# Kernel optimization log

Measured on AMD Instinct MI355X. Metric: run time of the kernel, lower is better.

Reference implementation:

```python
import jax, jax.numpy as jnp
import numpy as np

B = 262144
D = 16
G = 20000


def setup_inputs() -> dict:
    key = jax.random.key(0)
    ks = jax.random.split(key, 20)
    lin = lambda k, o, i: jax.random.normal(k, (o, i), jnp.float32) * (1.0 / np.sqrt(i))
    inp = {
        "x": jax.random.randint(ks[0], (B, 2), 0, G),
        "phenos": jax.random.normal(ks[1], (B, 2), jnp.float32),
        "emb": jax.random.normal(ks[2], (G, D), jnp.float32),
        "W1": lin(ks[3], D, D), "b1": jnp.zeros((D,), jnp.float32),
        "W2": lin(ks[4], D, D), "b2": jnp.zeros((D,), jnp.float32),
        "W3": lin(ks[5], D, D), "b3": jnp.zeros((D,), jnp.float32),
        # bilinear weights: small noise + stacked identity, as in the torch init
        "BW": 0.01 * jax.random.normal(ks[6], (D, D, D), jnp.float32)
              + jnp.broadcast_to(jnp.eye(D, dtype=jnp.float32)[None, :, :], (D, D, D)),
        "BD": 0.01 * jax.random.normal(ks[7], (D, D), jnp.float32) + 1.0,
        "Boff": 0.01 * jax.random.normal(ks[8], (D,), jnp.float32),
        "Wc1": lin(ks[9], D, D), "bc1": jnp.zeros((D,), jnp.float32),
        "Wc2": lin(ks[10], 1, D), "bc2": jnp.zeros((1,), jnp.float32),
    }
    return inp


def reference(x, phenos, emb, W1, b1, W2, b2, W3, b3, BW, BD, Boff, Wc1, bc1, Wc2, bc2):
    # embedding lookup: [B, 2, D] -> flatten gene axis into batch
    h = emb[x].reshape(-1, D)
    # embedding_ffn (dropout is identity in eval): Linear->ReLU->Linear->ReLU->Linear
    h = jax.nn.relu(h @ W1.T + b1)
    h = jax.nn.relu(h @ W2.T + b2)
    h = (h @ W3.T + b3).reshape(-1, 2, D)
    e0, e1 = h[:, 0, :], h[:, 1, :]  # [B, D] each
    # torch: x0 = BW.matmul(e0.T).T  -> x0[b,m,n] = sum_k BW[n,m,k] e0[b,k]
    A = jnp.einsum("nmk,bk->bmn", BW, e0)  # [B, D, D]
    # torch: x1 = BW.matmul(e1.T).T, *= BD, permute -> C[b,m,n] = sum_k BW[m,n,k] e1[b,k], scaled by BD[n,m]
    C = jnp.einsum("mnk,bk->bmn", BW, e1)  # [B, D, D]
    z = jnp.einsum("bmn,bmn,nm->bn", A, C, BD) + Boff  # [B, D]
    # embedding_comb: Linear->ReLU->Linear(D,1)
    z = jax.nn.relu(z @ Wc1.T + bc1)
    z = z @ Wc2.T + bc2  # [B, 1]
    return jnp.sum(phenos, axis=1) + z[:, 0]
```

## Files before the change

### kernel.cpp

```cpp
#include <hip/hip_runtime.h>

#define D  16
#define NB 262144
#define NG 20000
#define ROWPITCH 36

typedef __attribute__((ext_vector_type(8))) short bf16x8;
typedef __attribute__((ext_vector_type(4))) float f32x4;
typedef __attribute__((ext_vector_type(2))) float f32x2;
typedef __attribute__((ext_vector_type(2))) unsigned u32x2;

__device__ __forceinline__ unsigned pack_hi16(unsigned b0, unsigned b1) {
    return __builtin_amdgcn_perm(b1, b0, 0x07060302u);
}

__global__ void __launch_bounds__(256)
prep_kernel(const float* __restrict__ emb,
            const float* __restrict__ W1, const float* __restrict__ b1,
            const float* __restrict__ W2, const float* __restrict__ b2,
            const float* __restrict__ W3, const float* __restrict__ b3,
            const float* __restrict__ BW, const float* __restrict__ BD,
            const float* __restrict__ Wc1, const float* __restrict__ bc1,
            const float* __restrict__ Boff,
            float* __restrict__ T, short* __restrict__ Bhi, short* __restrict__ Blo,
            float* __restrict__ bc1p) {
    __shared__ float smem[8704];
    int tid = threadIdx.x;
    int blk = blockIdx.x;

    if (blk < 79) {
        int g = blk * 256 + tid;
        if (g >= NG) return;
        float h[D], t[D];
        const float4* ep = (const float4*)(emb + (size_t)g * D);
        float4 v0 = ep[0], v1 = ep[1], v2 = ep[2], v3 = ep[3];
        h[0]=v0.x; h[1]=v0.y; h[2]=v0.z; h[3]=v0.w;
        h[4]=v1.x; h[5]=v1.y; h[6]=v1.z; h[7]=v1.w;
        h[8]=v2.x; h[9]=v2.y; h[10]=v2.z; h[11]=v2.w;
        h[12]=v3.x; h[13]=v3.y; h[14]=v3.z; h[15]=v3.w;
        #pragma unroll
        for (int i = 0; i < D; ++i) {
            float a = b1[i];
            #pragma unroll
            for (int d = 0; d < D; ++d) a = fmaf(W1[i * D + d], h[d], a);
            t[i] = fmaxf(a, 0.f);
        }
        #pragma unroll
        for (int i = 0; i < D; ++i) {
            float a = b2[i];
            #pragma unroll
            for (int d = 0; d < D; ++d) a = fmaf(W2[i * D + d], t[d], a);
            h[i] = fmaxf(a, 0.f);
        }
        #pragma unroll
        for (int i = 0; i < D; ++i) {
            float a = b3[i];
            #pragma unroll
            for (int d = 0; d < D; ++d) a = fmaf(W3[i * D + d], h[d], a);
            t[i] = a;
        }
        float4* tp = (float4*)(T + (size_t)g * D);
        tp[0] = make_float4(t[0], t[1], t[2], t[3]);
        tp[1] = make_float4(t[4], t[5], t[6], t[7]);
        tp[2] = make_float4(t[8], t[9], t[10], t[11]);
        tp[3] = make_float4(t[12], t[13], t[14], t[15]);
        return;
    }

    float* bwS = smem;
    float* bdS = smem + 4096;
    float* MmS = smem + 4352;
    #pragma unroll
    for (int i = 0; i < 16; ++i) bwS[tid + 256 * i] = BW[tid + 256 * i];
    bdS[tid] = BD[tid];
    __syncthreads();

    int n = tid >> 4, j = tid & 15;
    float acc[16];
    #pragma unroll
    for (int k = 0; k < 16; ++k) acc[k] = 0.f;
    #pragma unroll
    for (int m = 0; m < 16; ++m) {
        float sw = bdS[n * 16 + m] * bwS[(m * 16 + n) * 16 + j];
        const f32x4* w1 = (const f32x4*)&bwS[(n * 16 + m) * 16];
        #pragma unroll
        for (int q = 0; q < 4; ++q) {
            f32x4 w = w1[q];
            acc[4 * q + 0] = fmaf(sw, w.x, acc[4 * q + 0]);
            acc[4 * q + 1] = fmaf(sw, w.y, acc[4 * q + 1]);
            acc[4 * q + 2] = fmaf(sw, w.z, acc[4 * q + 2]);
            acc[4 * q + 3] = fmaf(sw, w.w, acc[4 * q + 3]);
        }
    }
    #pragma unroll
    for (int k = 0; k < 16; ++k) MmS[(k * 16 + j) * 17 + n] = acc[k];
    __syncthreads();

    for (int idx = tid; idx < 512; idx += 256) {
        int s = idx >> 6, lane = idx & 63;
        int q = lane >> 4, nn = lane & 15;
        unsigned hw[4], lw[4];
        #pragma unroll
        for (int w = 0; w < 4; ++w) {
            int kk0 = s * 32 + q * 8 + 2 * w;
            float v0 = MmS[kk0 * 17 + nn], v1 = MmS[(kk0 + 1) * 17 + nn];
            unsigned b0 = __float_as_uint(v0), b1 = __float_as_uint(v1);
            float h0 = __uint_as_float(b0 & 0xFFFF0000u);
            float h1 = __uint_as_float(b1 & 0xFFFF0000u);
            hw[w] = pack_hi16(b0, b1);
            lw[w] = pack_hi16(__float_as_uint(v0 - h0), __float_as_uint(v1 - h1));
        }
        ((uint4*)Bhi)[idx] = make_uint4(hw[0], hw[1], hw[2], hw[3]);
        ((uint4*)Blo)[idx] = make_uint4(lw[0], lw[1], lw[2], lw[3]);
    }

    if (tid < 16) {
        float a = bc1[tid];
        #pragma unroll
        for (int nn = 0; nn < 16; ++nn) a += Wc1[tid * 16 + nn] * Boff[nn];
        bc1p[tid] = a;
    }
}

__global__ void __launch_bounds__(256)
main_kernel(const int* __restrict__ x, const float* __restrict__ phenos,
            const float* __restrict__ T,
            const short* __restrict__ Bhi, const short* __restrict__ Blo,
            const float* __restrict__ bc1p, const float* __restrict__ Wc1,
            const float* __restrict__ Wc2, const float* __restrict__ bc2,
            float* __restrict__ out) {
    __shared__ float smem[9216];
    int tid  = threadIdx.x;
    int wave = tid >> 6, lane = tid & 63;
    int quad = lane >> 4, nl = lane & 15;
    long base = (long)blockIdx.x * 256 + wave * 64;
    float* stg = smem + wave * 2304;

    bf16x8 bh[8], bl[8];
    #pragma unroll
    for (int s = 0; s < 8; ++s) {
        bh[s] = ((const bf16x8*)Bhi)[s * 64 + lane];
        bl[s] = ((const bf16x8*)Blo)[s * 64 + lane];
    }

    long r = base + lane;
    int2 g = ((const int2*)x)[r];
    {
        const f32x4* p0 = (const f32x4*)(T + g.x * 16);
        const f32x4* p1 = (const f32x4*)(T + g.y * 16);
        f32x4 c0 = p0[0], c1 = p0[1], c2 = p0[2], c3 = p0[3];
        f32x4 c4 = p1[0], c5 = p1[1], c6 = p1[2], c7 = p1[3];
        f32x4* wp = (f32x4*)(stg + lane * ROWPITCH);
        wp[0] = c0; wp[1] = c1; wp[2] = c2; wp[3] = c3;
        wp[4] = c4; wp[5] = c5; wp[6] = c6; wp[7] = c7;
    }
    __syncthreads();

    f32x4 acc[4];
    #pragma unroll
    for (int t = 0; t < 4; ++t) acc[t] = (f32x4){0.f, 0.f, 0.f, 0.f};
    const int par = quad >> 1;
    const int eo  = (quad & 1) * 8;

    #pragma unroll
    for (int t = 0; t < 4; ++t) {
        const float* rowp = stg + (t * 16 + nl) * ROWPITCH;
        float ev[8];
        #pragma unroll
        for (int s = 0; s < 8; ++s) ev[s] = rowp[2 * s + par];
        f32x4 e1a = *(const f32x4*)(rowp + 16 + eo);
        f32x4 e1b = *(const f32x4*)(rowp + 20 + eo);
        f32x2 e1p[4] = {(f32x2){e1a.x, e1a.y}, (f32x2){e1a.z, e1a.w},
                        (f32x2){e1b.x, e1b.y}, (f32x2){e1b.z, e1b.w}};

        #pragma unroll
        for (int s = 0; s < 8; ++s) {
            f32x2 evv = (f32x2){ev[s], ev[s]};
            unsigned aw[4], lw[4];
            #pragma unroll
            for (int w = 0; w < 4; ++w) {
                f32x2 p  = evv * e1p[w];
                u32x2 pb = __builtin_bit_cast(u32x2, p);
                u32x2 hb = pb & (u32x2){0xFFFF0000u, 0xFFFF0000u};
                f32x2 lo = p - __builtin_bit_cast(f32x2, hb);
                u32x2 lb = __builtin_bit_cast(u32x2, lo);
                aw[w] = pack_hi16(pb.x, pb.y);
                lw[w] = pack_hi16(lb.x, lb.y);
            }
            bf16x8 ah = __builtin_bit_cast(bf16x8, make_uint4(aw[0], aw[1], aw[2], aw[3]));
            bf16x8 al = __builtin_bit_cast(bf16x8, make_uint4(lw[0], lw[1], lw[2], lw[3]));
            acc[t] = __builtin_amdgcn_mfma_f32_16x16x32_bf16(ah, bh[s], acc[t], 0, 0, 0);
            acc[t] = __builtin_amdgcn_mfma_f32_16x16x32_bf16(ah, bl[s], acc[t], 0, 0, 0);
            acc[t] = __builtin_amdgcn_mfma_f32_16x16x32_bf16(al, bh[s], acc[t], 0, 0, 0);
        }
    }

    __syncthreads();
    float* zb = smem + wave * 1040;
    #pragma unroll
    for (int t = 0; t < 4; ++t) {
        #pragma unroll
        for (int reg = 0; reg < 4; ++reg)
            zb[nl * 65 + t * 16 + quad * 4 + reg] = acc[t][reg];
    }
    __syncthreads();

    float zv[16];
    #pragma unroll
    for (int n = 0; n < 16; ++n) zv[n] = zb[n * 65 + lane];

    float a2 = bc2[0];
    #pragma unroll
    for (int i = 0; i < 16; ++i) {
        float u = bc1p[i];
        #pragma unroll
        for (int n = 0; n < 16; ++n) u = fmaf(Wc1[i * 16 + n], zv[n], u);
        u = fmaxf(u, 0.f);
        a2 = fmaf(Wc2[i], u, a2);
    }

    float2 ph = ((const float2*)phenos)[r];
    out[r] = ph.x + ph.y + a2;
}

extern "C" void kernel_launch(void* const* d_in, const int* in_sizes, int n_in,
                              void* d_out, int out_size, void* d_ws, size_t ws_size,
                              hipStream_t stream) {
    const int*   x      = (const int*)  d_in[0];
    const float* phenos = (const float*)d_in[1];
    const float* emb    = (const float*)d_in[2];
    const float* W1     = (const float*)d_in[3];
    const float* b1     = (const float*)d_in[4];
    const float* W2     = (const float*)d_in[5];
    const float* b2     = (const float*)d_in[6];
    const float* W3     = (const float*)d_in[7];
    const float* b3     = (const float*)d_in[8];
    const float* BW     = (const float*)d_in[9];
    const float* BD     = (const float*)d_in[10];
    const float* Boff   = (const float*)d_in[11];
    const float* Wc1    = (const float*)d_in[12];
    const float* bc1    = (const float*)d_in[13];
    const float* Wc2    = (const float*)d_in[14];
    const float* bc2    = (const float*)d_in[15];
    float* out = (float*)d_out;

    char* wsb = (char*)d_ws;
    short* Bhi  = (short*)(wsb);
    short* Blo  = (short*)(wsb + 8192);
    float* bc1p = (float*)(wsb + 16384);
    float* T    = (float*)(wsb + 16448);

    prep_kernel<<<80, 256, 0, stream>>>(emb, W1, b1, W2, b2, W3, b3, BW, BD,
                                        Wc1, bc1, Boff, T, Bhi, Blo, bc1p);
    main_kernel<<<NB / 256, 256, 0, stream>>>(x, phenos, T, Bhi, Blo, bc1p, Wc1, Wc2, bc2, out);
}
```

Baseline: 112.8 us.

## Drop low-part MFMA term, round A operand to bf16, vectorize comb-layer matvec

Replaces the split hi/lo bf16 decomposition of the e0*e1 outer-product operand with a single round-to-nearest bf16 conversion. This removes one of three MFMAs per step and the lo-part arithmetic. The z staging buffer moves to a row-major layout with pitch 20, so each lane reads its 16 values with vector loads. The Wc1 matvec now uses packed float2 math. The change lowers accuracy, since the A operand now keeps only bf16 precision, which could exceed the tolerance.

```diff
diff --git a/kernel.cpp b/kernel.cpp
--- a/kernel.cpp
+++ b/kernel.cpp
@@ -1,14 +1,15 @@
 #include <hip/hip_runtime.h>
+#include <hip/hip_bf16.h>
 
 #define D  16
 #define NB 262144
 #define NG 20000
 #define ROWPITCH 36
+#define ZPITCH   20
 
 typedef __attribute__((ext_vector_type(8))) short bf16x8;
 typedef __attribute__((ext_vector_type(4))) float f32x4;
 typedef __attribute__((ext_vector_type(2))) float f32x2;
-typedef __attribute__((ext_vector_type(2))) unsigned u32x2;
 
 __device__ __forceinline__ unsigned pack_hi16(unsigned b0, unsigned b1) {
     return __builtin_amdgcn_perm(b1, b0, 0x07060302u);
@@ -170,51 +171,52 @@
         for (int s = 0; s < 8; ++s) ev[s] = rowp[2 * s + par];
         f32x4 e1a = *(const f32x4*)(rowp + 16 + eo);
         f32x4 e1b = *(const f32x4*)(rowp + 20 + eo);
-        f32x2 e1p[4] = {(f32x2){e1a.x, e1a.y}, (f32x2){e1a.z, e1a.w},
-                        (f32x2){e1b.x, e1b.y}, (f32x2){e1b.z, e1b.w}};
+        float2 e1p[4] = {make_float2(e1a.x, e1a.y), make_float2(e1a.z, e1a.w),
+                         make_float2(e1b.x, e1b.y), make_float2(e1b.z, e1b.w)};
 
         #pragma unroll
         for (int s = 0; s < 8; ++s) {
-            f32x2 evv = (f32x2){ev[s], ev[s]};
-            unsigned aw[4], lw[4];
+            unsigned aw[4];
             #pragma unroll
             for (int w = 0; w < 4; ++w) {
-                f32x2 p  = evv * e1p[w];
-                u32x2 pb = __builtin_bit_cast(u32x2, p);
-                u32x2 hb = pb & (u32x2){0xFFFF0000u, 0xFFFF0000u};
-                f32x2 lo = p - __builtin_bit_cast(f32x2, hb);
-                u32x2 lb = __builtin_bit_cast(u32x2, lo);
-                aw[w] = pack_hi16(pb.x, pb.y);
-                lw[w] = pack_hi16(lb.x, lb.y);
+                float2 p = make_float2(ev[s] * e1p[w].x, ev[s] * e1p[w].y);
+                __hip_bfloat162 hv = __float22bfloat162_rn(p);
+                aw[w] = *(unsigned*)&hv;
             }
             bf16x8 ah = __builtin_bit_cast(bf16x8, make_uint4(aw[0], aw[1], aw[2], aw[3]));
-            bf16x8 al = __builtin_bit_cast(bf16x8, make_uint4(lw[0], lw[1], lw[2], lw[3]));
             acc[t] = __builtin_amdgcn_mfma_f32_16x16x32_bf16(ah, bh[s], acc[t], 0, 0, 0);
             acc[t] = __builtin_amdgcn_mfma_f32_16x16x32_bf16(ah, bl[s], acc[t], 0, 0, 0);
-            acc[t] = __builtin_amdgcn_mfma_f32_16x16x32_bf16(al, bh[s], acc[t], 0, 0, 0);
-        }
-    }
-
-    __syncthreads();
-    float* zb = smem + wave * 1040;
+        }
+    }
+
+    __syncthreads();
+    float* zb = smem + wave * 1280;
     #pragma unroll
     for (int t = 0; t < 4; ++t) {
         #pragma unroll
         for (int reg = 0; reg < 4; ++reg)
-            zb[nl * 65 + t * 16 + quad * 4 + reg] = acc[t][reg];
-    }
-    __syncthreads();
-
-    float zv[16];
-    #pragma unroll
-    for (int n = 0; n < 16; ++n) zv[n] = zb[n * 65 + lane];
-
+            zb[(t * 16 + quad * 4 + reg) * ZPITCH + nl] = acc[t][reg];
+    }
+    __syncthreads();
+
+    const float* zr = zb + lane * ZPITCH;
+    f32x4 q0 = *(const f32x4*)(zr + 0);
+    f32x4 q1 = *(const f32x4*)(zr + 4);
+    f32x4 q2 = *(const f32x4*)(zr + 8);
+    f32x4 q3 = *(const f32x4*)(zr + 12);
+    f32x2 zv2[8] = {(f32x2){q0.x, q0.y}, (f32x2){q0.z, q0.w},
+                    (f32x2){q1.x, q1.y}, (f32x2){q1.z, q1.w},
+                    (f32x2){q2.x, q2.y}, (f32x2){q2.z, q2.w},
+                    (f32x2){q3.x, q3.y}, (f32x2){q3.z, q3.w}};
+
+    const f32x2* w2 = (const f32x2*)Wc1;
     float a2 = bc2[0];
     #pragma unroll
     for (int i = 0; i < 16; ++i) {
-        float u = bc1p[i];
-        #pragma unroll
-        for (int n = 0; n < 16; ++n) u = fmaf(Wc1[i * 16 + n], zv[n], u);
+        f32x2 u2 = (f32x2){0.f, 0.f};
+        #pragma unroll
+        for (int n2 = 0; n2 < 8; ++n2) u2 += w2[i * 8 + n2] * zv2[n2];
+        float u = u2.x + u2.y + bc1p[i];
         u = fmaxf(u, 0.f);
         a2 = fmaf(Wc2[i], u, a2);
     }
```

Result: faster. 105.8 us (-6.3%).
